# Optimization experiments

Measured on AMD Instinct MI355X. Metric: run time of the kernel, lower is better.

## Reference

```python
import jax, jax.numpy as jnp
import numpy as np

NX, NU, NY, NW = 64, 32, 32, 64
B, T = 256, 2048


def setup_inputs() -> dict:
    key = jax.random.key(0)
    ks = jax.random.split(key, 11)

    def lin_w(k, out_f, in_f):
        # torch.nn.Linear default init scale ~ 1/sqrt(in_f)
        lim = 1.0 / np.sqrt(in_f)
        return jax.random.uniform(k, (out_f, in_f), jnp.float32, -lim, lim)

    return {
        "x_pred": jax.random.normal(ks[0], (B, T, NU), jnp.float32),
        # Y initialized as identity in the module; keep it well-conditioned
        "Y": jnp.eye(NX, dtype=jnp.float32) + 0.01 * jax.random.normal(ks[1], (NX, NX), jnp.float32),
        # lambdas initialized to ones; keep strictly positive
        "lambdas": 1.0 + 0.1 * jax.random.uniform(ks[2], (NW, 1), jnp.float32),
        "A": lin_w(ks[3], NX, NX),
        "B1": lin_w(ks[4], NX, NU),
        "B2": lin_w(ks[5], NX, NW),
        "C1": lin_w(ks[6], NY, NX),
        "D11": lin_w(ks[7], NY, NU),
        "D12": lin_w(ks[8], NY, NW),
        "C2": lin_w(ks[9], NW, NX),
        "D21": lin_w(ks[10], NW, NU),
    }


def reference(x_pred, Y, lambdas, A, B1, B2, C1, D11, D12, C2, D21):
    n_batch, n_sample, _ = x_pred.shape
    nx = A.shape[0]
    Y_inv = jnp.linalg.inv(Y)
    t_inv = 1.0 / jnp.squeeze(lambdas)  # diag of T_inv, [nw]

    x0 = jnp.zeros((n_batch, nx), x_pred.dtype)
    u_seq = jnp.swapaxes(x_pred, 0, 1)  # [T, B, nu]

    def step(x, u):
        # z = (C2_tilde x + D21_tilde u) @ T_inv ; T_inv diagonal -> column scale
        z = (x @ C2.T + u @ D21.T) * t_inv
        w = jnp.tanh(z)
        y_k = x @ C1.T + u @ D11.T + w @ D12.T
        x_next = (x @ A.T + u @ B1.T + w @ B2.T) @ Y_inv
        return x_next, y_k

    x_final, ys = jax.lax.scan(step, x0, u_seq)
    y = jnp.swapaxes(ys, 0, 1)  # [B, T, ny]
    return y, x_final
```

## Files before the change

### kernel.cpp

```cpp
#include <hip/hip_runtime.h>
#include <cstddef>

#define NXS 64
#define NUS 32
#define NYS 32
#define NWS 64
#define BBATCH 256
#define TT  2048

#define SLP 20

typedef float v2f __attribute__((ext_vector_type(2)));

__device__ __forceinline__ float fast_tanh(float x) {
    float e = __expf(2.0f * x);
    return 1.0f - 2.0f * __builtin_amdgcn_rcpf(e + 1.0f);
}

template<int CTRL>
__device__ __forceinline__ float dpp_add(float v) {
    int t = __builtin_amdgcn_update_dpp(0, __float_as_int(v), CTRL, 0xF, 0xF, true);
    return v + __int_as_float(t);
}

__device__ __forceinline__ void step_barrier() {
    asm volatile("s_waitcnt lgkmcnt(0)\n\ts_barrier" ::: "memory");
}

__global__ __launch_bounds__(1024) void setup_g_kernel(const float* __restrict__ Y,
                                                       const float* __restrict__ lam,
                                                       const float* __restrict__ A,
                                                       const float* __restrict__ B1,
                                                       const float* __restrict__ B2,
                                                       const float* __restrict__ C1,
                                                       const float* __restrict__ D11,
                                                       const float* __restrict__ D12,
                                                       const float* __restrict__ C2,
                                                       const float* __restrict__ D21,
                                                       float* __restrict__ ws) {
    __shared__ float M[64 * 129];
    __shared__ float rowk[128];
    __shared__ float ck[64];
    __shared__ float WxT[160 * 64];
    const int tid = threadIdx.x;

    for (int idx = tid; idx < 64 * 64; idx += 1024) {
        int r = idx >> 6, c = idx & 63;
        M[r * 129 + c]      = Y[idx];
        M[r * 129 + 64 + c] = (r == c) ? 1.0f : 0.0f;
    }
    __syncthreads();

    for (int k = 0; k < 64; ++k) {
        float dv = 1.0f / M[k * 129 + k];
        if (tid < 128) rowk[tid] = M[k * 129 + tid] * dv;
        if (tid >= 128 && tid < 192) ck[tid - 128] = M[(tid - 128) * 129 + k];
        __syncthreads();
        for (int idx = tid; idx < 64 * 128; idx += 1024) {
            int r = idx >> 7, c = idx & 127;
            float cur = M[r * 129 + c];
            M[r * 129 + c] = (r == k) ? rowk[c] : cur - ck[r] * rowk[c];
        }
        __syncthreads();
    }

    for (int idx = tid; idx < 160 * 64; idx += 1024) {
        int k = idx >> 6, j = idx & 63;
        float s = 0.0f;
        if (k < 64) {
            #pragma unroll 8
            for (int m = 0; m < 64; ++m) s += A[m * 64 + k] * M[m * 129 + 64 + j];
        } else if (k < 96) {
            int ku = k - 64;
            #pragma unroll 8
            for (int m = 0; m < 64; ++m) s += B1[m * 32 + ku] * M[m * 129 + 64 + j];
        } else {
            int kw = k - 96;
            #pragma unroll 8
            for (int m = 0; m < 64; ++m) s += B2[m * 64 + kw] * M[m * 129 + 64 + j];
        }
        WxT[k * 64 + j] = s;
    }
    __syncthreads();

    for (int idx = tid; idx < 160 * 192; idx += 1024) {
        int c = idx / 192;
        int k = idx - c * 192;
        float v;
        if (c < 64) {
            if (k < 160) {
                int km = (k < 64) ? k : (k < 128) ? (96 + k - 64) : (64 + k - 128);
                float s = 0.0f;
                #pragma unroll 8
                for (int m = 0; m < 64; ++m) s += WxT[km * 64 + m] * C2[c * 64 + m];
                v = s / lam[c];
            } else {
                v = D21[c * 32 + (k - 160)] / lam[c];
            }
        } else if (c < 128) {
            int j = c - 64;
            if (k < 160) {
                int km = (k < 64) ? k : (k < 128) ? (96 + k - 64) : (64 + k - 128);
                v = WxT[km * 64 + j];
            } else v = 0.0f;
        } else {
            int j = c - 128;
            v = (k < 64)  ? C1[j * 64 + k]
              : (k < 128) ? D12[j * 64 + (k - 64)]
              : (k < 160) ? D11[j * 32 + (k - 128)]
                          : 0.0f;
        }
        ws[c * 192 + k] = v;
    }
}

__global__ __launch_bounds__(256, 1) void rnn6_kernel(const float* __restrict__ xp,
                                                      const float* __restrict__ ws,
                                                      float* __restrict__ out) {
    const int b   = blockIdx.x;
    const int tid = threadIdx.x;
    const int l   = tid & 63;
    const int wv  = tid >> 6;
    const int g   = l >> 3;
    const int e   = l & 7;
    const int Gq  = 8 * wv + g;

    __shared__ __align__(16) float sbuf[2][8][SLP];
    __shared__ __align__(16) float uRs[32][36];

    const float4* __restrict__ xp4 = (const float4*)(xp + (size_t)b * (TT * NUS));
    const size_t yb   = (size_t)b * (TT * NYS);
    const size_t xoff = (size_t)BBATCH * TT * NYS;

    v2f wst[5][8], wu4[5][4];
    #pragma unroll
    for (int r = 0; r < 5; ++r) {
        const float* Gc = ws + (size_t)(32 * r + Gq) * 192;
        const float* sb = Gc + 16 * e;
        #pragma unroll
        for (int k = 0; k < 4; ++k) {
            float4 gv = *(const float4*)(sb + 4 * k);
            wst[r][2 * k]     = (v2f){gv.x, gv.y};
            wst[r][2 * k + 1] = (v2f){gv.z, gv.w};
        }
        const float* ub = Gc + ((e < 4) ? (128 + 8 * e) : (160 + 8 * (e - 4)));
        #pragma unroll
        for (int t = 0; t < 2; ++t) {
            float4 gv = *(const float4*)(ub + 4 * t);
            wu4[r][2 * t]     = (v2f){gv.x, gv.y};
            wu4[r][2 * t + 1] = (v2f){gv.z, gv.w};
        }
    }

    {
        int s = tid >> 3, q8 = tid & 7;
        float4 v = make_float4(0.f, 0.f, 0.f, 0.f);
        if (s < 31) v = xp4[s * 8 + q8];
        *(float4*)&uRs[s][q8 * 4] = v;
        if (tid < 160) ((float*)sbuf)[tid] = 0.0f;
    }
    __syncthreads();

    const int wr_dim  = (e < 2) ? (64 + 32 * e + Gq) : (32 * (e - 2) + Gq);
    const int wr_off  = (wr_dim >> 4) * SLP + (wr_dim & 15);
    const bool wr_en   = (e < 4);
    const bool wr_tanh = (e < 2);

    float ybat[8];
    float lastx = 0.0f;
    float4 upref = make_float4(0.f, 0.f, 0.f, 0.f);

    auto dostep = [&](const float* __restrict__ Sr, float* __restrict__ Sw,
                      const float4* __restrict__ urow) -> float {
        const float4* sv4 = (const float4*)(Sr + e * SLP);
        float4 s0 = sv4[0], s1 = sv4[1], s2 = sv4[2], s3 = sv4[3];
        float4 u0 = urow[0], u1 = urow[1];
        float sr[5];
        #pragma unroll
        for (int r = 0; r < 5; ++r) {
            v2f a0 = (v2f){s0.x, s0.y} * wst[r][0] + (v2f){s1.x, s1.y} * wst[r][2];
            v2f a1 = (v2f){s0.z, s0.w} * wst[r][1] + (v2f){s1.z, s1.w} * wst[r][3];
            a0 += (v2f){s2.x, s2.y} * wst[r][4] + (v2f){s3.x, s3.y} * wst[r][6];
            a1 += (v2f){s2.z, s2.w} * wst[r][5] + (v2f){s3.z, s3.w} * wst[r][7];
            a0 += (v2f){u0.x, u0.y} * wu4[r][0] + (v2f){u1.x, u1.y} * wu4[r][2];
            a1 += (v2f){u0.z, u0.w} * wu4[r][1] + (v2f){u1.z, u1.w} * wu4[r][3];
            v2f a = a0 + a1;
            float s = a.x + a.y;
            s = dpp_add<0xB1>(s);
            s = dpp_add<0x4E>(s);
            s = dpp_add<0x141>(s);
            sr[r] = s;
        }
        float vA = (e == 0) ? sr[0] : sr[1];
        float vB = (e == 2) ? sr[2] : sr[3];
        float tv = fast_tanh(vA);
        float wval = wr_tanh ? tv : vB;
        if (wr_en) Sw[wr_off] = wval;
        lastx = vB;
        return sr[4];
    };

    {
        const float4* urow = (const float4*)((e < 4) ? &uRs[31][8 * e]
                                                     : &uRs[0][8 * (e - 4)]);
        (void)dostep((const float*)sbuf[0], (float*)sbuf[1], urow);
        step_barrier();
    }

    #pragma unroll 8
    for (int i = 0; i < TT; ++i) {
        const int rp = (i + 1) & 1, wp = i & 1;
        if ((i & 15) == 0) {
            int t = i + 16 + (tid >> 3);
            if (tid < 128 && t < TT) upref = xp4[t * 8 + (tid & 7)];
        }
        if ((i & 15) == 8) {
            int t = i + 8 + (tid >> 3);
            if (tid < 128 && t < TT) *(float4*)&uRs[t & 31][(tid & 7) * 4] = upref;
        }
        const int ip = i & 31, ic = (i + 1) & 31;
        const float4* urow = (const float4*)((e < 4) ? &uRs[ip][8 * e]
                                                     : &uRs[ic][8 * (e - 4)]);
        float yd = dostep((const float*)sbuf[rp], (float*)sbuf[wp], urow);
        ybat[i & 7] = yd;
        if ((i & 7) == 7 && e == 4) {
            size_t base = yb + (size_t)(i - 7) * NYS + Gq;
            #pragma unroll
            for (int ss = 0; ss < 8; ++ss) out[base + (size_t)ss * NYS] = ybat[ss];
        }
        step_barrier();
    }

    if (e == 2 || e == 3)
        out[xoff + (size_t)b * 64 + wr_dim] = lastx;
}

extern "C" void kernel_launch(void* const* d_in, const int* in_sizes, int n_in,
                              void* d_out, int out_size, void* d_ws, size_t ws_size,
                              hipStream_t stream) {
    const float* xp  = (const float*)d_in[0];
    const float* Y   = (const float*)d_in[1];
    const float* lam = (const float*)d_in[2];
    const float* A   = (const float*)d_in[3];
    const float* B1  = (const float*)d_in[4];
    const float* B2  = (const float*)d_in[5];
    const float* C1  = (const float*)d_in[6];
    const float* D11 = (const float*)d_in[7];
    const float* D12 = (const float*)d_in[8];
    const float* C2  = (const float*)d_in[9];
    const float* D21 = (const float*)d_in[10];
    float* out = (float*)d_out;
    float* ws  = (float*)d_ws;

    hipLaunchKernelGGL(setup_g_kernel, dim3(1), dim3(1024), 0, stream,
                       Y, lam, A, B1, B2, C1, D11, D12, C2, D21, ws);
    hipLaunchKernelGGL(rnn6_kernel, dim3(BBATCH), dim3(256), 0, stream, xp, ws, out);
}
```

Before: 1.097 ms.

## Spread recurrent step over 512 threads with fewer outputs per thread

The recurrent kernel now runs 512 threads per batch row instead of 256, so each 8-lane group computes at most three output columns (z, x, y) instead of five. This shortens the serial per-step dot-product chain, and an explicit packed-FMA helper accumulates each column. The one-block setup kernel is also split into three launches, one of which spreads the weight-matrix products over 16 blocks. The cost is that each step's barrier now synchronises eight waves instead of four, and there are extra kernel launches.

```diff
diff --git a/kernel.cpp b/kernel.cpp
--- a/kernel.cpp
+++ b/kernel.cpp
@@ -8,7 +8,7 @@
 #define BBATCH 256
 #define TT  2048
 
-#define SLP 20
+#define WS_YSTG 24576
 
 typedef float v2f __attribute__((ext_vector_type(2)));
 
@@ -23,25 +23,19 @@
     return v + __int_as_float(t);
 }
 
+__device__ __forceinline__ void pk_fma(v2f& acc, v2f x, v2f w) {
+    asm("v_pk_fma_f32 %0, %1, %2, %0" : "+v"(acc) : "v"(x), "v"(w));
+}
+
 __device__ __forceinline__ void step_barrier() {
     asm volatile("s_waitcnt lgkmcnt(0)\n\ts_barrier" ::: "memory");
 }
 
-__global__ __launch_bounds__(1024) void setup_g_kernel(const float* __restrict__ Y,
-                                                       const float* __restrict__ lam,
-                                                       const float* __restrict__ A,
-                                                       const float* __restrict__ B1,
-                                                       const float* __restrict__ B2,
-                                                       const float* __restrict__ C1,
-                                                       const float* __restrict__ D11,
-                                                       const float* __restrict__ D12,
-                                                       const float* __restrict__ C2,
-                                                       const float* __restrict__ D21,
-                                                       float* __restrict__ ws) {
+__global__ __launch_bounds__(1024) void setup_inv_kernel(const float* __restrict__ Y,
+                                                         float* __restrict__ ws) {
     __shared__ float M[64 * 129];
     __shared__ float rowk[128];
     __shared__ float ck[64];
-    __shared__ float WxT[160 * 64];
     const int tid = threadIdx.x;
 
     for (int idx = tid; idx < 64 * 64; idx += 1024) {
@@ -63,33 +57,53 @@
         }
         __syncthreads();
     }
-
-    for (int idx = tid; idx < 160 * 64; idx += 1024) {
+    for (int idx = tid; idx < 4096; idx += 1024) {
+        int r = idx >> 6, c = idx & 63;
+        ws[WS_YSTG + idx] = M[r * 129 + 64 + c];
+    }
+}
+
+__global__ __launch_bounds__(256) void setup_gxw_kernel(const float* __restrict__ lam,
+                                                        const float* __restrict__ A,
+                                                        const float* __restrict__ B1,
+                                                        const float* __restrict__ B2,
+                                                        const float* __restrict__ C2,
+                                                        const float* __restrict__ D21,
+                                                        float* __restrict__ ws) {
+    __shared__ float Yi[64 * 64];
+    __shared__ float WxT[160 * 64];
+    const int tid = threadIdx.x;
+    const int bid = blockIdx.x;
+
+    for (int idx = tid; idx < 4096; idx += 256) Yi[idx] = ws[WS_YSTG + idx];
+    __syncthreads();
+
+    for (int idx = tid; idx < 10240; idx += 256) {
         int k = idx >> 6, j = idx & 63;
         float s = 0.0f;
         if (k < 64) {
             #pragma unroll 8
-            for (int m = 0; m < 64; ++m) s += A[m * 64 + k] * M[m * 129 + 64 + j];
+            for (int m = 0; m < 64; ++m) s += A[m * 64 + k] * Yi[m * 64 + j];
         } else if (k < 96) {
             int ku = k - 64;
             #pragma unroll 8
-            for (int m = 0; m < 64; ++m) s += B1[m * 32 + ku] * M[m * 129 + 64 + j];
+            for (int m = 0; m < 64; ++m) s += B1[m * 32 + ku] * Yi[m * 64 + j];
         } else {
             int kw = k - 96;
             #pragma unroll 8
-            for (int m = 0; m < 64; ++m) s += B2[m * 64 + kw] * M[m * 129 + 64 + j];
-        }
-        WxT[k * 64 + j] = s;
-    }
-    __syncthreads();
-
-    for (int idx = tid; idx < 160 * 192; idx += 1024) {
+            for (int m = 0; m < 64; ++m) s += B2[m * 64 + kw] * Yi[m * 64 + j];
+        }
+        WxT[idx] = s;
+    }
+    __syncthreads();
+
+    for (int idx = bid * 1536 + tid; idx < bid * 1536 + 1536; idx += 256) {
         int c = idx / 192;
         int k = idx - c * 192;
+        int km = (k < 64) ? k : (k < 128) ? (96 + k - 64) : (64 + k - 128);
         float v;
         if (c < 64) {
             if (k < 160) {
-                int km = (k < 64) ? k : (k < 128) ? (96 + k - 64) : (64 + k - 128);
                 float s = 0.0f;
                 #pragma unroll 8
                 for (int m = 0; m < 64; ++m) s += WxT[km * 64 + m] * C2[c * 64 + m];
@@ -97,115 +111,119 @@
             } else {
                 v = D21[c * 32 + (k - 160)] / lam[c];
             }
-        } else if (c < 128) {
+        } else {
             int j = c - 64;
-            if (k < 160) {
-                int km = (k < 64) ? k : (k < 128) ? (96 + k - 64) : (64 + k - 128);
-                v = WxT[km * 64 + j];
-            } else v = 0.0f;
-        } else {
-            int j = c - 128;
-            v = (k < 64)  ? C1[j * 64 + k]
-              : (k < 128) ? D12[j * 64 + (k - 64)]
-              : (k < 160) ? D11[j * 32 + (k - 128)]
-                          : 0.0f;
+            v = (k < 160) ? WxT[km * 64 + j] : 0.0f;
         }
         ws[c * 192 + k] = v;
     }
 }
 
-__global__ __launch_bounds__(256, 1) void rnn6_kernel(const float* __restrict__ xp,
+__global__ __launch_bounds__(256) void setup_y_kernel(const float* __restrict__ C1,
+                                                      const float* __restrict__ D11,
+                                                      const float* __restrict__ D12,
+                                                      float* __restrict__ ws) {
+    for (int idx = blockIdx.x * 256 + threadIdx.x; idx < 6144; idx += 16 * 256) {
+        int c = 128 + idx / 192;
+        int k = idx % 192;
+        int j = c - 128;
+        float v = (k < 64)  ? C1[j * 64 + k]
+                : (k < 128) ? D12[j * 64 + (k - 64)]
+                : (k < 160) ? D11[j * 32 + (k - 128)]
+                            : 0.0f;
+        ws[c * 192 + k] = v;
+    }
+}
+
+__global__ __launch_bounds__(512, 2) void rnn7_kernel(const float* __restrict__ xp,
                                                       const float* __restrict__ ws,
                                                       float* __restrict__ out) {
     const int b   = blockIdx.x;
     const int tid = threadIdx.x;
-    const int l   = tid & 63;
-    const int wv  = tid >> 6;
-    const int g   = l >> 3;
-    const int e   = l & 7;
-    const int Gq  = 8 * wv + g;
-
-    __shared__ __align__(16) float sbuf[2][8][SLP];
+
+    __shared__ __align__(16) float sbuf[2][160];
     __shared__ __align__(16) float uRs[32][36];
 
     const float4* __restrict__ xp4 = (const float4*)(xp + (size_t)b * (TT * NUS));
     const size_t yb   = (size_t)b * (TT * NYS);
     const size_t xoff = (size_t)BBATCH * TT * NYS;
 
-    v2f wst[5][8], wu4[5][4];
+    if (tid < 256) {
+        int s = tid >> 3, q8 = tid & 7;
+        float4 v = make_float4(0.f, 0.f, 0.f, 0.f);
+        if (s < 31) v = xp4[s * 8 + q8];
+        *(float4*)&uRs[s][q8 * 4] = v;
+    }
+    if (tid < 160) sbuf[0][tid] = 0.0f;
+    __syncthreads();
+
+    const int e  = tid & 7;
+    const int Gq = tid >> 3;
+
+    const int NOUT = (Gq < 32) ? 3 : 2;
+    v2f w[3][12];
     #pragma unroll
-    for (int r = 0; r < 5; ++r) {
-        const float* Gc = ws + (size_t)(32 * r + Gq) * 192;
+    for (int r = 0; r < 3; ++r) {
+        if (r >= NOUT) break;
+        const int col = (r == 0) ? Gq : (r == 1) ? (64 + Gq) : (128 + Gq);
+        const float* Gc = ws + (size_t)col * 192;
         const float* sb = Gc + 16 * e;
         #pragma unroll
         for (int k = 0; k < 4; ++k) {
             float4 gv = *(const float4*)(sb + 4 * k);
-            wst[r][2 * k]     = (v2f){gv.x, gv.y};
-            wst[r][2 * k + 1] = (v2f){gv.z, gv.w};
+            w[r][2 * k]     = (v2f){gv.x, gv.y};
+            w[r][2 * k + 1] = (v2f){gv.z, gv.w};
         }
         const float* ub = Gc + ((e < 4) ? (128 + 8 * e) : (160 + 8 * (e - 4)));
         #pragma unroll
         for (int t = 0; t < 2; ++t) {
             float4 gv = *(const float4*)(ub + 4 * t);
-            wu4[r][2 * t]     = (v2f){gv.x, gv.y};
-            wu4[r][2 * t + 1] = (v2f){gv.z, gv.w};
-        }
-    }
-
-    {
-        int s = tid >> 3, q8 = tid & 7;
-        float4 v = make_float4(0.f, 0.f, 0.f, 0.f);
-        if (s < 31) v = xp4[s * 8 + q8];
-        *(float4*)&uRs[s][q8 * 4] = v;
-        if (tid < 160) ((float*)sbuf)[tid] = 0.0f;
-    }
-    __syncthreads();
-
-    const int wr_dim  = (e < 2) ? (64 + 32 * e + Gq) : (32 * (e - 2) + Gq);
-    const int wr_off  = (wr_dim >> 4) * SLP + (wr_dim & 15);
-    const bool wr_en   = (e < 4);
-    const bool wr_tanh = (e < 2);
+            w[r][8 + 2 * t] = (v2f){gv.x, gv.y};
+            w[r][9 + 2 * t] = (v2f){gv.z, gv.w};
+        }
+    }
+
+    const int wr_off = (e == 0) ? (((64 + Gq) >> 4) * 20 + ((64 + Gq) & 15))
+                                : ((Gq >> 4) * 20 + (Gq & 15));
 
     float ybat[8];
     float lastx = 0.0f;
     float4 upref = make_float4(0.f, 0.f, 0.f, 0.f);
 
-    auto dostep = [&](const float* __restrict__ Sr, float* __restrict__ Sw,
-                      const float4* __restrict__ urow) -> float {
-        const float4* sv4 = (const float4*)(Sr + e * SLP);
+    auto dostep = [&](int rb, int wb, int ip, int ic,
+                      float& s0o, float& s1o, float& s2o) {
+        const float4* sv4 = (const float4*)(&sbuf[rb][0] + e * 20);
         float4 s0 = sv4[0], s1 = sv4[1], s2 = sv4[2], s3 = sv4[3];
-        float4 u0 = urow[0], u1 = urow[1];
-        float sr[5];
+        const float4* uu = (const float4*)&uRs[(e < 4) ? ip : ic][8 * (e & 3)];
+        float4 u0 = uu[0], u1 = uu[1];
+        v2f sv[12] = {{s0.x, s0.y}, {s0.z, s0.w}, {s1.x, s1.y}, {s1.z, s1.w},
+                      {s2.x, s2.y}, {s2.z, s2.w}, {s3.x, s3.y}, {s3.z, s3.w},
+                      {u0.x, u0.y}, {u0.z, u0.w}, {u1.x, u1.y}, {u1.z, u1.w}};
+        float sr[3] = {0.f, 0.f, 0.f};
         #pragma unroll
-        for (int r = 0; r < 5; ++r) {
-            v2f a0 = (v2f){s0.x, s0.y} * wst[r][0] + (v2f){s1.x, s1.y} * wst[r][2];
-            v2f a1 = (v2f){s0.z, s0.w} * wst[r][1] + (v2f){s1.z, s1.w} * wst[r][3];
-            a0 += (v2f){s2.x, s2.y} * wst[r][4] + (v2f){s3.x, s3.y} * wst[r][6];
-            a1 += (v2f){s2.z, s2.w} * wst[r][5] + (v2f){s3.z, s3.w} * wst[r][7];
-            a0 += (v2f){u0.x, u0.y} * wu4[r][0] + (v2f){u1.x, u1.y} * wu4[r][2];
-            a1 += (v2f){u0.z, u0.w} * wu4[r][1] + (v2f){u1.z, u1.w} * wu4[r][3];
-            v2f a = a0 + a1;
-            float s = a.x + a.y;
+        for (int r = 0; r < 3; ++r) {
+            if (r >= NOUT) break;
+            v2f acc = (v2f){0.f, 0.f};
+            #pragma unroll
+            for (int k = 0; k < 12; ++k) pk_fma(acc, sv[k], w[r][k]);
+            float s = acc.x + acc.y;
             s = dpp_add<0xB1>(s);
             s = dpp_add<0x4E>(s);
             s = dpp_add<0x141>(s);
             sr[r] = s;
         }
-        float vA = (e == 0) ? sr[0] : sr[1];
-        float vB = (e == 2) ? sr[2] : sr[3];
-        float tv = fast_tanh(vA);
-        float wval = wr_tanh ? tv : vB;
-        if (wr_en) Sw[wr_off] = wval;
-        lastx = vB;
-        return sr[4];
+        if (e < 2) {
+            float val = (e == 0) ? fast_tanh(sr[0]) : sr[1];
+            sbuf[wb][wr_off] = val;
+        }
+        s0o = sr[0]; s1o = sr[1]; s2o = sr[2];
     };
 
     {
-        const float4* urow = (const float4*)((e < 4) ? &uRs[31][8 * e]
-                                                     : &uRs[0][8 * (e - 4)]);
-        (void)dostep((const float*)sbuf[0], (float*)sbuf[1], urow);
-        step_barrier();
-    }
+        float a, bv, c;
+        dostep(0, 1, 31, 0, a, bv, c);
+    }
+    step_barrier();
 
     #pragma unroll 8
     for (int i = 0; i < TT; ++i) {
@@ -218,21 +236,21 @@
             int t = i + 8 + (tid >> 3);
             if (tid < 128 && t < TT) *(float4*)&uRs[t & 31][(tid & 7) * 4] = upref;
         }
-        const int ip = i & 31, ic = (i + 1) & 31;
-        const float4* urow = (const float4*)((e < 4) ? &uRs[ip][8 * e]
-                                                     : &uRs[ic][8 * (e - 4)]);
-        float yd = dostep((const float*)sbuf[rp], (float*)sbuf[wp], urow);
-        ybat[i & 7] = yd;
-        if ((i & 7) == 7 && e == 4) {
-            size_t base = yb + (size_t)(i - 7) * NYS + Gq;
-            #pragma unroll
-            for (int ss = 0; ss < 8; ++ss) out[base + (size_t)ss * NYS] = ybat[ss];
+        float sr0, sr1, sr2;
+        dostep(rp, wp, i & 31, (i + 1) & 31, sr0, sr1, sr2);
+        lastx = sr1;
+        if (NOUT == 3 && e == 2) {
+            ybat[i & 7] = sr2;
+            if ((i & 7) == 7) {
+                size_t base = yb + (size_t)(i - 7) * NYS + Gq;
+                #pragma unroll
+                for (int ss = 0; ss < 8; ++ss) out[base + (size_t)ss * NYS] = ybat[ss];
+            }
         }
         step_barrier();
     }
 
-    if (e == 2 || e == 3)
-        out[xoff + (size_t)b * 64 + wr_dim] = lastx;
+    if (e == 1) out[xoff + (size_t)b * 64 + Gq] = lastx;
 }
 
 extern "C" void kernel_launch(void* const* d_in, const int* in_sizes, int n_in,
@@ -252,7 +270,10 @@
     float* out = (float*)d_out;
     float* ws  = (float*)d_ws;
 
-    hipLaunchKernelGGL(setup_g_kernel, dim3(1), dim3(1024), 0, stream,
-                       Y, lam, A, B1, B2, C1, D11, D12, C2, D21, ws);
-    hipLaunchKernelGGL(rnn6_kernel, dim3(BBATCH), dim3(256), 0, stream, xp, ws, out);
-}
+    hipLaunchKernelGGL(setup_inv_kernel, dim3(1),  dim3(1024), 0, stream, Y, ws);
+    hipLaunchKernelGGL(setup_gxw_kernel, dim3(16), dim3(256),  0, stream,
+                       lam, A, B1, B2, C2, D21, ws);
+    hipLaunchKernelGGL(setup_y_kernel,   dim3(16), dim3(256),  0, stream,
+                       C1, D11, D12, ws);
+    hipLaunchKernelGGL(rnn7_kernel, dim3(BBATCH), dim3(512), 0, stream, xp, ws, out);
+}
```

New measurement: 916.7 us. 1.2x faster.
